# Kernel tuning notes

Hardware: AMD Instinct MI355X
Metric: run time of the kernel (lower is better)

The kernel has to match this reference:

```python
import jax, jax.numpy as jnp
import numpy as np

N_EMBED = 1024
N_HEADS = 16
HEAD = N_EMBED // N_HEADS
EPS = 1e-5


def setup_inputs() -> dict:
    key = jax.random.key(0)
    ks = jax.random.split(key, 16)
    C = N_EMBED
    s = lambda fan_in: 1.0 / np.sqrt(fan_in)
    return {
        "x": jax.random.normal(ks[0], (4, 2048, C), jnp.float32),
        "ln1_g": jnp.ones((C,), jnp.float32),
        "ln1_b": jnp.zeros((C,), jnp.float32),
        "w_attn": jax.random.normal(ks[1], (C, 3 * C), jnp.float32) * s(C),
        "b_attn": jnp.zeros((3 * C,), jnp.float32),
        "w_proj": jax.random.normal(ks[2], (C, C), jnp.float32) * s(C),
        "b_proj": jnp.zeros((C,), jnp.float32),
        "ln2_g": jnp.ones((C,), jnp.float32),
        "ln2_b": jnp.zeros((C,), jnp.float32),
        "w_fc": jax.random.normal(ks[3], (C, 4 * C), jnp.float32) * s(C),
        "b_fc": jnp.zeros((4 * C,), jnp.float32),
        "w_fc2": jax.random.normal(ks[4], (4 * C, C), jnp.float32) * s(4 * C),
        "b_fc2": jnp.zeros((C,), jnp.float32),
    }


def _layernorm(x, g, b):
    mu = jnp.mean(x, axis=-1, keepdims=True)
    var = jnp.mean(jnp.square(x - mu), axis=-1, keepdims=True)
    return (x - mu) * jax.lax.rsqrt(var + EPS) * g + b


def _attention(x, w_attn, b_attn, w_proj, b_proj):
    B, T, C = x.shape
    qkv = x @ w_attn + b_attn  # [B,T,3C]
    q, k, v = jnp.split(qkv, 3, axis=-1)
    q = q.reshape(B, T, N_HEADS, HEAD).transpose(0, 2, 1, 3)  # [B,H,T,D]
    k = k.reshape(B, T, N_HEADS, HEAD).transpose(0, 2, 1, 3)
    v = v.reshape(B, T, N_HEADS, HEAD).transpose(0, 2, 1, 3)
    scale = 1.0 / np.sqrt(HEAD)
    affin = jnp.einsum("bhqd,bhkd->bhqk", q, k) * scale  # [B,H,T,T]
    causal = jnp.tril(jnp.ones((T, T), bool))
    affin = jnp.where(causal, affin, -jnp.inf)
    affin = jax.nn.softmax(affin, axis=-1)
    y = jnp.einsum("bhqk,bhkd->bhqd", affin, v)  # [B,H,T,D]
    y = y.transpose(0, 2, 1, 3).reshape(B, T, C)
    return y @ w_proj + b_proj


def reference(x, ln1_g, ln1_b, w_attn, b_attn, w_proj, b_proj,
              ln2_g, ln2_b, w_fc, b_fc, w_fc2, b_fc2):
    x = x + _attention(_layernorm(x, ln1_g, ln1_b), w_attn, b_attn, w_proj, b_proj)
    h = _layernorm(x, ln2_g, ln2_b)
    h = jax.nn.gelu(h @ w_fc + b_fc, approximate=True)  # tanh GELU
    x = x + (h @ w_fc2 + b_fc2)
    return x
```

## Files before the change

### kernel.cpp

```cpp
#include <hip/hip_runtime.h>
#include <math.h>


#define M_ROWS 8192
#define T_SEQ 2048
#define N_EMB 1024
#define N_HEADS 16
#define HEAD_D 64

typedef _Float16 f16;
typedef __attribute__((ext_vector_type(8))) _Float16 f16x8;
typedef __attribute__((ext_vector_type(4))) _Float16 f16x4;
typedef __attribute__((ext_vector_type(4))) float f32x4;

__device__ __forceinline__ void async16(void* lds, const void* g) {
    __builtin_amdgcn_global_load_lds(
        (const __attribute__((address_space(1))) unsigned int*)g,
        (__attribute__((address_space(3))) unsigned int*)lds, 16, 0, 0);
}

__device__ __forceinline__ float gelu_tanh(float v) {
    float u = 0.7978845608028654f * (v + 0.044715f * v * v * v);
    float e = __expf(2.0f * u);
    float t = 1.0f - 2.0f / (e + 1.0f);
    return 0.5f * v * (1.0f + t);
}

__launch_bounds__(256)
__global__ void wconv_kernel(const float* __restrict__ W, f16* __restrict__ WT,
                             int K, int N) {
    __shared__ float t[32][33];
    int tx = threadIdx.x & 31, ty = threadIdx.x >> 5;
    int n0 = blockIdx.x * 32, k0 = blockIdx.y * 32;
    #pragma unroll
    for (int r = 0; r < 4; r++)
        t[ty * 4 + r][tx] = W[(size_t)(k0 + ty * 4 + r) * N + n0 + tx];
    __syncthreads();
    #pragma unroll
    for (int r = 0; r < 4; r++)
        WT[(size_t)(n0 + ty * 4 + r) * K + k0 + tx] = (f16)t[tx][ty * 4 + r];
}

__launch_bounds__(256)
__global__ void ln_kernel(const float* __restrict__ x, const float* __restrict__ g,
                          const float* __restrict__ b, f16* __restrict__ y) {
    int row = blockIdx.x;
    int tid = threadIdx.x;
    const float* xr = x + (size_t)row * N_EMB;
    float4 v = *(const float4*)(xr + tid * 4);
    float s  = v.x + v.y + v.z + v.w;
    float sq = v.x * v.x + v.y * v.y + v.z * v.z + v.w * v.w;
    #pragma unroll
    for (int off = 32; off > 0; off >>= 1) {
        s  += __shfl_down(s, off);
        sq += __shfl_down(sq, off);
    }
    __shared__ float ws_[4], wq_[4];
    __shared__ float mean_s, rstd_s;
    int lane = tid & 63, wid = tid >> 6;
    if (lane == 0) { ws_[wid] = s; wq_[wid] = sq; }
    __syncthreads();
    if (tid == 0) {
        float st = ws_[0] + ws_[1] + ws_[2] + ws_[3];
        float qt = wq_[0] + wq_[1] + wq_[2] + wq_[3];
        float mu = st * (1.0f / N_EMB);
        float var = qt * (1.0f / N_EMB) - mu * mu;
        mean_s = mu;
        rstd_s = rsqrtf(var + 1e-5f);
    }
    __syncthreads();
    float mu = mean_s, r = rstd_s;
    float4 gv = *(const float4*)(g + tid * 4);
    float4 bv = *(const float4*)(b + tid * 4);
    f16x4 o;
    o.x = (f16)((v.x - mu) * r * gv.x + bv.x);
    o.y = (f16)((v.y - mu) * r * gv.y + bv.y);
    o.z = (f16)((v.z - mu) * r * gv.z + bv.z);
    o.w = (f16)((v.w - mu) * r * gv.w + bv.w);
    *(f16x4*)(y + (size_t)row * N_EMB + tid * 4) = o;
}

template <int EPI>
__launch_bounds__(256, 2)
__global__ void gemm_f16(const f16* __restrict__ A, const f16* __restrict__ Bt,
                         const float* __restrict__ bias, const float* __restrict__ res,
                         float* __restrict__ Cf, f16* __restrict__ Ch,
                         f16* __restrict__ vT, int K, int N) {
    __shared__ f16 As[3][256 * 32];
    __shared__ f16 Bs[3][128 * 32];
    int tid = threadIdx.x;
    int lane = tid & 63, wave = tid >> 6;
    int wr = wave >> 1, wc = wave & 1;
    int quad = lane >> 4, l16 = lane & 15;

    int nx = gridDim.x;
    int nwg = nx * gridDim.y;
    int orig = blockIdx.y * nx + blockIdx.x;
    int cpx = nwg >> 3;
    int swz = (orig & 7) * cpx + (orig >> 3);
    int m0 = (swz / nx) * 256, n0 = (swz % nx) * 128;

    int srow = tid >> 2;
    int sg = (tid & 3) ^ (srow & 3);
    const f16* pA = A  + (size_t)(m0 + srow) * K + sg * 8;
    const f16* pB = Bt + (size_t)(n0 + srow) * K + sg * 8;
    char* dA = (char*)As + (size_t)tid * 16;
    char* dB = (char*)Bs + (size_t)tid * 16;

    int nt = K >> 5;

    #pragma unroll
    for (int r = 0; r < 4; r++) async16(dA + r * 4096, pA + (size_t)(r * 64) * K);
    #pragma unroll
    for (int r = 0; r < 2; r++) async16(dB + r * 4096, pB + (size_t)(r * 64) * K);
    #pragma unroll
    for (int r = 0; r < 4; r++) async16(dA + 16384 + r * 4096, pA + (size_t)(r * 64) * K + 32);
    #pragma unroll
    for (int r = 0; r < 2; r++) async16(dB + 8192  + r * 4096, pB + (size_t)(r * 64) * K + 32);

    f32x4 acc[8][4] = {};
    int cswz = (quad ^ (l16 & 3)) * 8;
    int bufr = 0;
    for (int t = 0; t < nt; t++) {
        if (t + 1 < nt) asm volatile("s_waitcnt vmcnt(6)" ::: "memory");
        else            asm volatile("s_waitcnt vmcnt(0)" ::: "memory");
        __builtin_amdgcn_s_barrier();

        const f16* as = As[bufr];
        const f16* bs = Bs[bufr];
        int bn = bufr + 2 >= 3 ? bufr - 1 : bufr + 2;
        bool pf = (t + 2 < nt);
        size_t koff = (size_t)(t + 2) * 32;

        f16x8 bf[4];
        #pragma unroll
        for (int j = 0; j < 4; j++)
            bf[j] = *(const f16x8*)&bs[(wc * 64 + j * 16 + l16) * 32 + cswz];

        if (pf) {
            async16(dA + bn * 16384,        pA + koff);
            async16(dA + bn * 16384 + 4096, pA + (size_t)64 * K + koff);
            async16(dA + bn * 16384 + 8192, pA + (size_t)128 * K + koff);
        }
        f16x8 af[4];
        #pragma unroll
        for (int i = 0; i < 4; i++)
            af[i] = *(const f16x8*)&as[(wr * 128 + i * 16 + l16) * 32 + cswz];
        __builtin_amdgcn_s_setprio(1);
        #pragma unroll
        for (int i = 0; i < 4; i++)
            #pragma unroll
            for (int j = 0; j < 4; j++)
                acc[i][j] = __builtin_amdgcn_mfma_f32_16x16x32_f16(
                    af[i], bf[j], acc[i][j], 0, 0, 0);
        __builtin_amdgcn_s_setprio(0);

        if (pf) {
            async16(dA + bn * 16384 + 12288, pA + (size_t)192 * K + koff);
            async16(dB + bn * 8192,          pB + koff);
            async16(dB + bn * 8192 + 4096,   pB + (size_t)64 * K + koff);
        }
        #pragma unroll
        for (int i = 0; i < 4; i++)
            af[i] = *(const f16x8*)&as[(wr * 128 + (4 + i) * 16 + l16) * 32 + cswz];
        __builtin_amdgcn_s_setprio(1);
        #pragma unroll
        for (int i = 0; i < 4; i++)
            #pragma unroll
            for (int j = 0; j < 4; j++)
                acc[4 + i][j] = __builtin_amdgcn_mfma_f32_16x16x32_f16(
                    af[i], bf[j], acc[4 + i][j], 0, 0, 0);
        __builtin_amdgcn_s_setprio(0);

        bufr = bufr + 1 >= 3 ? 0 : bufr + 1;
    }

    #pragma unroll
    for (int i = 0; i < 8; i++) {
        int row0 = m0 + wr * 128 + i * 16 + quad * 4;
        #pragma unroll
        for (int j = 0; j < 4; j++) {
            int col = n0 + wc * 64 + j * 16 + l16;
            float bb = bias[col];
            if (EPI == 3) {
                if (n0 < 2048) {
                    #pragma unroll
                    for (int r = 0; r < 4; r++)
                        Ch[(size_t)(row0 + r) * 2048 + col] = (f16)(acc[i][j][r] + bb);
                } else {
                    int hh = (col - 2048) >> 6, dd = col & 63;
                    int bb_ = row0 >> 11, t0 = row0 & 2047;
                    f16x4 pk;
                    pk.x = (f16)(acc[i][j][0] + bb);
                    pk.y = (f16)(acc[i][j][1] + bb);
                    pk.z = (f16)(acc[i][j][2] + bb);
                    pk.w = (f16)(acc[i][j][3] + bb);
                    *(f16x4*)(vT + ((size_t)(bb_ * 16 + hh) * 64 + dd) * 2048 + t0) = pk;
                }
            } else {
                #pragma unroll
                for (int r = 0; r < 4; r++) {
                    size_t idx = (size_t)(row0 + r) * N + col;
                    float v = acc[i][j][r] + bb;
                    if (EPI == 1) v += res[idx];
                    if (EPI == 2) Ch[idx] = (f16)gelu_tanh(v);
                    else          Cf[idx] = v;
                }
            }
        }
    }
}

__launch_bounds__(256, 2)
__global__ void flash_kernel(const f16* __restrict__ qk, const f16* __restrict__ vT,
                             f16* __restrict__ y) {
    __shared__ __align__(16) char smem[67584];
    f16* Ks = (f16*)smem;
    f16* Vs = (f16*)(smem + 16384);
    int tid = threadIdx.x;
    int lane = tid & 63, w = tid >> 6;
    int quad = lane >> 4, l16 = lane & 15;
    f16* Ps = (f16*)(smem + 32768 + w * 8704);

    int bh = blockIdx.y;
    int b = bh >> 4, h = bh & 15;

    for (int half = 0; half < 2; half++) {
        int qt = half ? (int)blockIdx.x : 15 - (int)blockIdx.x;
        int q0 = qt * 128;

        f16x8 qf[2][2];
        #pragma unroll
        for (int qn = 0; qn < 2; qn++) {
            int q = q0 + w * 32 + qn * 16 + l16;
            #pragma unroll
            for (int dblk = 0; dblk < 2; dblk++) {
                f16x8 t = *(const f16x8*)(qk + (size_t)(b * T_SEQ + q) * 2048 +
                                          h * 64 + dblk * 32 + quad * 8);
                #pragma unroll
                for (int e = 0; e < 8; e++) t[e] = t[e] * (f16)0.125f;
                qf[qn][dblk] = t;
            }
        }

        float m_r[2] = {-INFINITY, -INFINITY};
        float l_r[2] = {0.0f, 0.0f};
        f32x4 Oacc[2][4] = {};

        for (int jt = 0; jt <= qt; jt++) {
            int j0 = jt * 128;
            __syncthreads();
            #pragma unroll
            for (int i = 0; i < 4; i++) {
                int L = i * 256 + tid;
                int j = L >> 3, g1 = L & 7;
                int g = g1 ^ (j & 7);
                async16((char*)Ks + (size_t)L * 16,
                        qk + (size_t)(b * T_SEQ + j0 + j) * 2048 + 1024 + h * 64 + g * 8);
            }
            #pragma unroll
            for (int i = 0; i < 4; i++) {
                int L = i * 256 + tid;
                int d = L >> 4, g1 = L & 15;
                int g = (g1 & 8) | ((g1 ^ d) & 7);
                async16((char*)Vs + (size_t)L * 16,
                        vT + ((size_t)(bh) * 64 + d) * 2048 + j0 + g * 8);
            }
            __syncthreads();

            f32x4 S[8][2];
            #pragma unroll
            for (int jm = 0; jm < 8; jm++) {
                f16x8 kf[2];
                #pragma unroll
                for (int dblk = 0; dblk < 2; dblk++) {
                    int j = jm * 16 + l16;
                    int g = (dblk * 4 + quad) ^ (j & 7);
                    kf[dblk] = *(const f16x8*)(Ks + (size_t)(j * 8 + g) * 8);
                }
                #pragma unroll
                for (int qn = 0; qn < 2; qn++) {
                    f32x4 s = {};
                    s = __builtin_amdgcn_mfma_f32_16x16x32_f16(kf[0], qf[qn][0], s, 0, 0, 0);
                    s = __builtin_amdgcn_mfma_f32_16x16x32_f16(kf[1], qf[qn][1], s, 0, 0, 0);
                    S[jm][qn] = s;
                }
            }

            if (jt == qt) {
                #pragma unroll
                for (int jm = 0; jm < 8; jm++)
                    #pragma unroll
                    for (int qn = 0; qn < 2; qn++)
                        #pragma unroll
                        for (int r = 0; r < 4; r++) {
                            int jl = jm * 16 + quad * 4 + r;
                            int ql = w * 32 + qn * 16 + l16;
                            if (jl > ql) S[jm][qn][r] = -1e30f;
                        }
            }

            float alpha[2];
            #pragma unroll
            for (int qn = 0; qn < 2; qn++) {
                float tmax = -INFINITY;
                #pragma unroll
                for (int jm = 0; jm < 8; jm++)
                    #pragma unroll
                    for (int r = 0; r < 4; r++)
                        tmax = fmaxf(tmax, S[jm][qn][r]);
                tmax = fmaxf(tmax, __shfl_xor(tmax, 16));
                tmax = fmaxf(tmax, __shfl_xor(tmax, 32));
                float mnew = fmaxf(m_r[qn], tmax);
                alpha[qn] = __expf(m_r[qn] - mnew);
                m_r[qn] = mnew;
                float rsum = 0.0f;
                #pragma unroll
                for (int jm = 0; jm < 8; jm++)
                    #pragma unroll
                    for (int r = 0; r < 4; r++) {
                        float p = __expf(S[jm][qn][r] - mnew);
                        S[jm][qn][r] = p;
                        rsum += p;
                    }
                rsum += __shfl_xor(rsum, 16);
                rsum += __shfl_xor(rsum, 32);
                l_r[qn] = l_r[qn] * alpha[qn] + rsum;
            }

            #pragma unroll
            for (int jm = 0; jm < 8; jm++)
                #pragma unroll
                for (int qn = 0; qn < 2; qn++) {
                    f16x4 pk;
                    pk.x = (f16)S[jm][qn][0];
                    pk.y = (f16)S[jm][qn][1];
                    pk.z = (f16)S[jm][qn][2];
                    pk.w = (f16)S[jm][qn][3];
                    *(f16x4*)(Ps + (size_t)(qn * 16 + l16) * 136 + jm * 16 + quad * 4) = pk;
                }

            float aPV[2][4];
            #pragma unroll
            for (int m = 0; m < 2; m++)
                #pragma unroll
                for (int r = 0; r < 4; r++)
                    aPV[m][r] = __shfl(alpha[m], quad * 20 + r);
            #pragma unroll
            for (int m = 0; m < 2; m++)
                #pragma unroll
                for (int n = 0; n < 4; n++)
                    #pragma unroll
                    for (int r = 0; r < 4; r++)
                        Oacc[m][n][r] *= aPV[m][r];

            #pragma unroll
            for (int kblk = 0; kblk < 4; kblk++) {
                f16x8 pf[2];
                #pragma unroll
                for (int m = 0; m < 2; m++)
                    pf[m] = *(const f16x8*)(Ps + (size_t)(m * 16 + l16) * 136 +
                                            kblk * 32 + quad * 8);
                f16x8 vf[4];
                #pragma unroll
                for (int n = 0; n < 4; n++) {
                    int d = n * 16 + l16;
                    int g = (kblk * 4 + quad);
                    int gs = (g & 8) | ((g ^ d) & 7);
                    vf[n] = *(const f16x8*)(Vs + (size_t)(d * 16 + gs) * 8);
                }
                #pragma unroll
                for (int m = 0; m < 2; m++)
                    #pragma unroll
                    for (int n = 0; n < 4; n++)
                        Oacc[m][n] = __builtin_amdgcn_mfma_f32_16x16x32_f16(
                            pf[m], vf[n], Oacc[m][n], 0, 0, 0);
            }
        }

        #pragma unroll
        for (int m = 0; m < 2; m++) {
            float lPV[4];
            #pragma unroll
            for (int r = 0; r < 4; r++)
                lPV[r] = 1.0f / __shfl(l_r[m], quad * 20 + r);
            #pragma unroll
            for (int n = 0; n < 4; n++) {
                #pragma unroll
                for (int r = 0; r < 4; r++) {
                    int q = q0 + w * 32 + m * 16 + quad * 4 + r;
                    y[(size_t)(b * T_SEQ + q) * N_EMB + h * 64 + n * 16 + l16] =
                        (f16)(Oacc[m][n][r] * lPV[r]);
                }
            }
        }
    }
}

extern "C" void kernel_launch(void* const* d_in, const int* in_sizes, int n_in,
                              void* d_out, int out_size, void* d_ws, size_t ws_size,
                              hipStream_t stream) {
    const float* x      = (const float*)d_in[0];
    const float* ln1_g  = (const float*)d_in[1];
    const float* ln1_b  = (const float*)d_in[2];
    const float* w_attn = (const float*)d_in[3];
    const float* b_attn = (const float*)d_in[4];
    const float* w_proj = (const float*)d_in[5];
    const float* b_proj = (const float*)d_in[6];
    const float* ln2_g  = (const float*)d_in[7];
    const float* ln2_b  = (const float*)d_in[8];
    const float* w_fc   = (const float*)d_in[9];
    const float* b_fc   = (const float*)d_in[10];
    const float* w_fc2  = (const float*)d_in[11];
    const float* b_fc2  = (const float*)d_in[12];
    float* out = (float*)d_out;

    const size_t MB = 1024 * 1024;
    char* ws = (char*)d_ws;
    f16*   lnbuf = (f16*)ws;
    f16*   qkbuf = (f16*)(ws + 16 * MB);
    f16*   vTbuf = (f16*)(ws + 48 * MB);
    f16*   ybuf  = (f16*)(ws + 64 * MB);
    f16*   h     = (f16*)(ws + 80 * MB);
    f16*   wT    = (f16*)(ws + 144 * MB);
    f16* wT_attn = wT;
    f16* wT_proj = wT_attn + (size_t)3072 * 1024;
    f16* wT_fc   = wT_proj + (size_t)1024 * 1024;
    f16* wT_fc2  = wT_fc   + (size_t)1024 * 4096;

    wconv_kernel<<<dim3(3072 / 32, 1024 / 32), 256, 0, stream>>>(w_attn, wT_attn, 1024, 3072);
    wconv_kernel<<<dim3(1024 / 32, 1024 / 32), 256, 0, stream>>>(w_proj, wT_proj, 1024, 1024);
    wconv_kernel<<<dim3(4096 / 32, 1024 / 32), 256, 0, stream>>>(w_fc,   wT_fc,   1024, 4096);
    wconv_kernel<<<dim3(1024 / 32, 4096 / 32), 256, 0, stream>>>(w_fc2,  wT_fc2,  4096, 1024);

    ln_kernel<<<M_ROWS, 256, 0, stream>>>(x, ln1_g, ln1_b, lnbuf);
    gemm_f16<3><<<dim3(3072 / 128, M_ROWS / 256), 256, 0, stream>>>(
        lnbuf, wT_attn, b_attn, nullptr, nullptr, qkbuf, vTbuf, 1024, 3072);
    flash_kernel<<<dim3(8, 64), 256, 0, stream>>>(qkbuf, vTbuf, ybuf);
    gemm_f16<1><<<dim3(1024 / 128, M_ROWS / 256), 256, 0, stream>>>(
        ybuf, wT_proj, b_proj, x, out, nullptr, nullptr, 1024, 1024);
    ln_kernel<<<M_ROWS, 256, 0, stream>>>(out, ln2_g, ln2_b, lnbuf);
    gemm_f16<2><<<dim3(4096 / 128, M_ROWS / 256), 256, 0, stream>>>(
        lnbuf, wT_fc, b_fc, nullptr, nullptr, h, nullptr, 1024, 4096);
    gemm_f16<1><<<dim3(1024 / 128, M_ROWS / 256), 256, 0, stream>>>(
        h, wT_fc2, b_fc2, out, out, nullptr, nullptr, 4096, 1024);
}
```

Before: 591.7 us.

## Rewrite GEMM as 8-wave 256x256 tile kernel with K=64 double buffering

```diff
diff --git a/kernel.cpp b/kernel.cpp
--- a/kernel.cpp
+++ b/kernel.cpp
@@ -80,107 +80,166 @@
     *(f16x4*)(y + (size_t)row * N_EMB + tid * 4) = o;
 }
 
-template <int EPI>
-__launch_bounds__(256, 2)
-__global__ void gemm_f16(const f16* __restrict__ A, const f16* __restrict__ Bt,
-                         const float* __restrict__ bias, const float* __restrict__ res,
-                         float* __restrict__ Cf, f16* __restrict__ Ch,
-                         f16* __restrict__ vT, int K, int N) {
-    __shared__ f16 As[3][256 * 32];
-    __shared__ f16 Bs[3][128 * 32];
+template <int EPI, int BM, int BN>
+__launch_bounds__(512, 2)
+__global__ void gemm8(const f16* __restrict__ A, const f16* __restrict__ Bt,
+                      const float* __restrict__ bias, const float* __restrict__ res,
+                      float* __restrict__ Cf, f16* __restrict__ Ch,
+                      f16* __restrict__ vT, int K, int N) {
+    constexpr int MI = BM / 32;
+    constexpr int MH = MI / 2;
+    constexpr int NJ = BN / 64;
+    constexpr int AROUNDS = BM / 64;
+    constexpr int BROUNDS = BN / 64;
+    constexpr int ROUNDS = AROUNDS + BROUNDS;
+    constexpr int P1E = (ROUNDS == 8) ? 3 : 2;
+    constexpr int P2E = (ROUNDS == 8) ? 6 : 4;
+    __shared__ f16 As[2][BM * 64];
+    __shared__ f16 Bs[2][BN * 64];
+
     int tid = threadIdx.x;
     int lane = tid & 63, wave = tid >> 6;
-    int wr = wave >> 1, wc = wave & 1;
+    int wr = wave >> 2, wc = wave & 3;
     int quad = lane >> 4, l16 = lane & 15;
 
-    int nx = gridDim.x;
-    int nwg = nx * gridDim.y;
+    int nx = gridDim.x, nwg = nx * gridDim.y;
     int orig = blockIdx.y * nx + blockIdx.x;
     int cpx = nwg >> 3;
     int swz = (orig & 7) * cpx + (orig >> 3);
-    int m0 = (swz / nx) * 256, n0 = (swz % nx) * 128;
-
-    int srow = tid >> 2;
-    int sg = (tid & 3) ^ (srow & 3);
-    const f16* pA = A  + (size_t)(m0 + srow) * K + sg * 8;
-    const f16* pB = Bt + (size_t)(n0 + srow) * K + sg * 8;
-    char* dA = (char*)As + (size_t)tid * 16;
-    char* dB = (char*)Bs + (size_t)tid * 16;
-
-    int nt = K >> 5;
-
-    #pragma unroll
-    for (int r = 0; r < 4; r++) async16(dA + r * 4096, pA + (size_t)(r * 64) * K);
-    #pragma unroll
-    for (int r = 0; r < 2; r++) async16(dB + r * 4096, pB + (size_t)(r * 64) * K);
-    #pragma unroll
-    for (int r = 0; r < 4; r++) async16(dA + 16384 + r * 4096, pA + (size_t)(r * 64) * K + 32);
-    #pragma unroll
-    for (int r = 0; r < 2; r++) async16(dB + 8192  + r * 4096, pB + (size_t)(r * 64) * K + 32);
-
-    f32x4 acc[8][4] = {};
-    int cswz = (quad ^ (l16 & 3)) * 8;
-    int bufr = 0;
+    int m0 = (swz / nx) * BM, n0 = (swz % nx) * BN;
+
+    int srow = tid >> 3;
+    int sglog = (tid & 7) ^ (srow & 7);
+    const f16* pa[AROUNDS];
+    const f16* pb[BROUNDS];
+    #pragma unroll
+    for (int r = 0; r < AROUNDS; r++)
+        pa[r] = A + (size_t)(m0 + r * 64 + srow) * K + sglog * 8;
+    #pragma unroll
+    for (int r = 0; r < BROUNDS; r++)
+        pb[r] = Bt + (size_t)(n0 + r * 64 + srow) * K + sglog * 8;
+
+    int nt = K >> 6;
+
+    auto stage = [&](int t, int buf, int r) {
+        if (r < AROUNDS)
+            async16((char*)As[buf] + (size_t)(r * 512 + tid) * 16,
+                    pa[r] + (size_t)t * 64);
+        else
+            async16((char*)Bs[buf] + (size_t)((r - AROUNDS) * 512 + tid) * 16,
+                    pb[r - AROUNDS] + (size_t)t * 64);
+    };
+
+    #pragma unroll
+    for (int r = 0; r < ROUNDS; r++) stage(0, 0, r);
+
+    f32x4 acc[MI][NJ] = {};
     for (int t = 0; t < nt; t++) {
-        if (t + 1 < nt) asm volatile("s_waitcnt vmcnt(6)" ::: "memory");
-        else            asm volatile("s_waitcnt vmcnt(0)" ::: "memory");
+        int p = t & 1;
+        asm volatile("s_waitcnt vmcnt(0)" ::: "memory");
         __builtin_amdgcn_s_barrier();
-
-        const f16* as = As[bufr];
-        const f16* bs = Bs[bufr];
-        int bn = bufr + 2 >= 3 ? bufr - 1 : bufr + 2;
-        bool pf = (t + 2 < nt);
-        size_t koff = (size_t)(t + 2) * 32;
-
-        f16x8 bf[4];
-        #pragma unroll
-        for (int j = 0; j < 4; j++)
-            bf[j] = *(const f16x8*)&bs[(wc * 64 + j * 16 + l16) * 32 + cswz];
+        const f16* as = As[p];
+        const f16* bs = Bs[p];
+        bool pf = (t + 1 < nt);
+        f16x8 a0[MH], a1[MH], b0[NJ], b1[NJ];
 
         if (pf) {
-            async16(dA + bn * 16384,        pA + koff);
-            async16(dA + bn * 16384 + 4096, pA + (size_t)64 * K + koff);
-            async16(dA + bn * 16384 + 8192, pA + (size_t)128 * K + koff);
-        }
-        f16x8 af[4];
-        #pragma unroll
-        for (int i = 0; i < 4; i++)
-            af[i] = *(const f16x8*)&as[(wr * 128 + i * 16 + l16) * 32 + cswz];
+            #pragma unroll
+            for (int r = 0; r < P1E; r++) stage(t + 1, p ^ 1, r);
+        }
+        #pragma unroll
+        for (int i = 0; i < MH; i++) {
+            int row = wr * (BM / 2) + i * 16 + l16;
+            a0[i] = *(const f16x8*)&as[row * 64 + ((quad) ^ (row & 7)) * 8];
+        }
+        #pragma unroll
+        for (int j = 0; j < NJ; j++) {
+            int row = wc * (BN / 4) + j * 16 + l16;
+            b0[j] = *(const f16x8*)&bs[row * 64 + ((quad) ^ (row & 7)) * 8];
+        }
+        asm volatile("s_waitcnt lgkmcnt(0)" ::: "memory");
         __builtin_amdgcn_s_setprio(1);
         #pragma unroll
-        for (int i = 0; i < 4; i++)
-            #pragma unroll
-            for (int j = 0; j < 4; j++)
+        for (int i = 0; i < MH; i++) {
+            #pragma unroll
+            for (int j = 0; j < NJ; j++)
                 acc[i][j] = __builtin_amdgcn_mfma_f32_16x16x32_f16(
-                    af[i], bf[j], acc[i][j], 0, 0, 0);
+                    a0[i], b0[j], acc[i][j], 0, 0, 0);
+        }
         __builtin_amdgcn_s_setprio(0);
+        __builtin_amdgcn_s_barrier();
 
         if (pf) {
-            async16(dA + bn * 16384 + 12288, pA + (size_t)192 * K + koff);
-            async16(dB + bn * 8192,          pB + koff);
-            async16(dB + bn * 8192 + 4096,   pB + (size_t)64 * K + koff);
-        }
-        #pragma unroll
-        for (int i = 0; i < 4; i++)
-            af[i] = *(const f16x8*)&as[(wr * 128 + (4 + i) * 16 + l16) * 32 + cswz];
+            #pragma unroll
+            for (int r = P1E; r < P2E; r++) stage(t + 1, p ^ 1, r);
+        }
+        #pragma unroll
+        for (int i = 0; i < MH; i++) {
+            int row = wr * (BM / 2) + (MH + i) * 16 + l16;
+            a1[i] = *(const f16x8*)&as[row * 64 + ((quad) ^ (row & 7)) * 8];
+        }
+        asm volatile("s_waitcnt lgkmcnt(0)" ::: "memory");
         __builtin_amdgcn_s_setprio(1);
         #pragma unroll
-        for (int i = 0; i < 4; i++)
-            #pragma unroll
-            for (int j = 0; j < 4; j++)
-                acc[4 + i][j] = __builtin_amdgcn_mfma_f32_16x16x32_f16(
-                    af[i], bf[j], acc[4 + i][j], 0, 0, 0);
+        for (int i = 0; i < MH; i++) {
+            #pragma unroll
+            for (int j = 0; j < NJ; j++)
+                acc[MH + i][j] = __builtin_amdgcn_mfma_f32_16x16x32_f16(
+                    a1[i], b0[j], acc[MH + i][j], 0, 0, 0);
+        }
         __builtin_amdgcn_s_setprio(0);
-
-        bufr = bufr + 1 >= 3 ? 0 : bufr + 1;
+        __builtin_amdgcn_s_barrier();
+
+        if (pf) {
+            #pragma unroll
+            for (int r = P2E; r < ROUNDS; r++) stage(t + 1, p ^ 1, r);
+        }
+        #pragma unroll
+        for (int i = 0; i < MH; i++) {
+            int row = wr * (BM / 2) + i * 16 + l16;
+            a0[i] = *(const f16x8*)&as[row * 64 + ((4 + quad) ^ (row & 7)) * 8];
+        }
+        #pragma unroll
+        for (int j = 0; j < NJ; j++) {
+            int row = wc * (BN / 4) + j * 16 + l16;
+            b1[j] = *(const f16x8*)&bs[row * 64 + ((4 + quad) ^ (row & 7)) * 8];
+        }
+        asm volatile("s_waitcnt lgkmcnt(0)" ::: "memory");
+        __builtin_amdgcn_s_setprio(1);
+        #pragma unroll
+        for (int i = 0; i < MH; i++) {
+            #pragma unroll
+            for (int j = 0; j < NJ; j++)
+                acc[i][j] = __builtin_amdgcn_mfma_f32_16x16x32_f16(
+                    a0[i], b1[j], acc[i][j], 0, 0, 0);
+        }
+        __builtin_amdgcn_s_setprio(0);
+        __builtin_amdgcn_s_barrier();
+
+        #pragma unroll
+        for (int i = 0; i < MH; i++) {
+            int row = wr * (BM / 2) + (MH + i) * 16 + l16;
+            a1[i] = *(const f16x8*)&as[row * 64 + ((4 + quad) ^ (row & 7)) * 8];
+        }
+        asm volatile("s_waitcnt lgkmcnt(0)" ::: "memory");
+        __builtin_amdgcn_s_setprio(1);
+        #pragma unroll
+        for (int i = 0; i < MH; i++) {
+            #pragma unroll
+            for (int j = 0; j < NJ; j++)
+                acc[MH + i][j] = __builtin_amdgcn_mfma_f32_16x16x32_f16(
+                    a1[i], b1[j], acc[MH + i][j], 0, 0, 0);
+        }
+        __builtin_amdgcn_s_setprio(0);
+        __builtin_amdgcn_s_barrier();
     }
 
     #pragma unroll
-    for (int i = 0; i < 8; i++) {
-        int row0 = m0 + wr * 128 + i * 16 + quad * 4;
-        #pragma unroll
-        for (int j = 0; j < 4; j++) {
-            int col = n0 + wc * 64 + j * 16 + l16;
+    for (int i = 0; i < MI; i++) {
+        int row0 = m0 + wr * (BM / 2) + i * 16 + quad * 4;
+        #pragma unroll
+        for (int j = 0; j < NJ; j++) {
+            int col = n0 + wc * (BN / 4) + j * 16 + l16;
             float bb = bias[col];
             if (EPI == 3) {
                 if (n0 < 2048) {
@@ -434,14 +493,14 @@
     wconv_kernel<<<dim3(1024 / 32, 4096 / 32), 256, 0, stream>>>(w_fc2,  wT_fc2,  4096, 1024);
 
     ln_kernel<<<M_ROWS, 256, 0, stream>>>(x, ln1_g, ln1_b, lnbuf);
-    gemm_f16<3><<<dim3(3072 / 128, M_ROWS / 256), 256, 0, stream>>>(
+    gemm8<3, 256, 256><<<dim3(3072 / 256, M_ROWS / 256), 512, 0, stream>>>(
         lnbuf, wT_attn, b_attn, nullptr, nullptr, qkbuf, vTbuf, 1024, 3072);
     flash_kernel<<<dim3(8, 64), 256, 0, stream>>>(qkbuf, vTbuf, ybuf);
-    gemm_f16<1><<<dim3(1024 / 128, M_ROWS / 256), 256, 0, stream>>>(
+    gemm8<1, 128, 256><<<dim3(1024 / 256, M_ROWS / 128), 512, 0, stream>>>(
         ybuf, wT_proj, b_proj, x, out, nullptr, nullptr, 1024, 1024);
     ln_kernel<<<M_ROWS, 256, 0, stream>>>(out, ln2_g, ln2_b, lnbuf);
-    gemm_f16<2><<<dim3(4096 / 128, M_ROWS / 256), 256, 0, stream>>>(
+    gemm8<2, 256, 256><<<dim3(4096 / 256, M_ROWS / 256), 512, 0, stream>>>(
         lnbuf, wT_fc, b_fc, nullptr, nullptr, h, nullptr, 1024, 4096);
-    gemm_f16<1><<<dim3(1024 / 128, M_ROWS / 256), 256, 0, stream>>>(
+    gemm8<1, 128, 256><<<dim3(1024 / 256, M_ROWS / 128), 512, 0, stream>>>(
         h, wT_fc2, b_fc2, out, out, nullptr, nullptr, 4096, 1024);
 }
```

Result: no change. 587.2 us (-0.8%).
